# Kernel tuning notes

Measured on AMD Instinct MI355X. Metric: run time of the kernel, lower is better.

## Reference

```python
import jax, jax.numpy as jnp
import numpy as np

# pywt db2 analysis filters, reversed as in pytorch_wavelets.prep_filt_afb1d
# (torch conv1d is cross-correlation, so reversed filter == true convolution)
_H0 = np.array([0.48296291314469025, 0.8365163037378079,
                0.22414386804185735, -0.12940952255092145], dtype=np.float32)  # lowpass
_H1 = np.array([-0.12940952255092145, -0.22414386804185735,
                0.8365163037378079, -0.48296291314469025], dtype=np.float32)   # highpass


def setup_inputs() -> dict:
    key = jax.random.key(0)
    x = jax.random.normal(key, (16, 256, 128, 128), dtype=jnp.float32)
    return {"x": x}


def _dwt_channel(x):
    """1-level db2 DWT (mode='zero') along channel axis of x: (B, C, H, W).

    Equivalent to looping DWT1DForward over every (h, w) pixel, keeping the
    first C//2 low-pass coeffs in channels [:C//2] and the first C//2
    high-pass coeffs in channels [C//2:].
    """
    B, C, H, W = x.shape
    h0 = jnp.asarray(_H0, dtype=x.dtype)
    h1 = jnp.asarray(_H1, dtype=x.dtype)
    xt = jnp.moveaxis(x, 1, -1)                       # (B, H, W, C)
    # zero-mode padding: L=4, even C -> pad 2 each side (p = 4)
    xp = jnp.pad(xt, ((0, 0), (0, 0), (0, 0), (2, 2)))
    # output coeff k uses xp[..., 2k + t], t = 0..3; keep k = 0..C//2-1
    def filt(h):
        return sum(h[t] * jax.lax.slice_in_dim(xp, t, t + C - 1, stride=2, axis=3)
                   for t in range(4))                 # (B, H, W, C//2)
    lo = filt(h0)
    hi = filt(h1)
    out = jnp.concatenate([lo, hi], axis=-1)          # (B, H, W, C)
    return jnp.moveaxis(out, -1, 1)                   # (B, C, H, W)


def reference(x):
    return _dwt_channel(x)
```

## Files before the change

kernel.cpp:

```cpp
#include <hip/hip_runtime.h>

#define H00  0.48296291314469025f
#define H01  0.8365163037378079f
#define H02  0.22414386804185735f
#define H03 -0.12940952255092145f

#define H10 -0.12940952255092145f
#define H11 -0.22414386804185735f
#define H12  0.8365163037378079f
#define H13 -0.48296291314469025f

typedef float f4 __attribute__((ext_vector_type(4)));

namespace {
constexpr int Bn      = 16;
constexpr int Cn      = 256;
constexpr int HWv     = (128 * 128) / 4;
constexpr int KPAIRS  = Cn / 2;
constexpr int KPC     = 16;
constexpr int NCHUNK  = KPAIRS / KPC;
constexpr unsigned SPATIAL4 = (unsigned)Bn * HWv;
}

__global__ __launch_bounds__(256, 8) void dwt_db2_channel_kernel(
    const f4* __restrict__ x, f4* __restrict__ out)
{
    const unsigned tid   = blockIdx.x * 256u + threadIdx.x;
    const unsigned s4    = tid & (SPATIAL4 - 1);
    const unsigned chunk = tid >> 16;
    const unsigned b     = s4 / HWv;
    const unsigned hw    = s4 & (HWv - 1);
    const int      k0    = chunk * KPC;

    const f4* __restrict__ xp  = x   + (size_t)b * Cn * HWv + hw
                                     + (size_t)(2 * k0) * HWv;
    f4*       __restrict__ olo = out + (size_t)b * Cn * HWv + hw
                                     + (size_t)k0 * HWv;
    f4*       __restrict__ ohi = olo + (size_t)KPAIRS * HWv;

    f4 w0, w1;
    if (chunk == 0) {
        w0 = (f4){0.f, 0.f, 0.f, 0.f};
        w1 = w0;
    } else {
        w0 = __builtin_nontemporal_load(xp - 2 * HWv);
        w1 = __builtin_nontemporal_load(xp - 1 * HWv);
    }

#pragma unroll 2
    for (int kk = 0; kk < KPC; ++kk) {
        const f4 w2 = __builtin_nontemporal_load(xp);
        const f4 w3 = __builtin_nontemporal_load(xp + HWv);
        xp += 2 * HWv;

        f4 lo = H00 * w0 + H01 * w1 + H02 * w2 + H03 * w3;
        f4 hi = H10 * w0 + H11 * w1 + H12 * w2 + H13 * w3;

        __builtin_nontemporal_store(lo, olo);
        __builtin_nontemporal_store(hi, ohi);
        olo += HWv;
        ohi += HWv;

        w0 = w2;
        w1 = w3;
    }
}

extern "C" void kernel_launch(void* const* d_in, const int* in_sizes, int n_in,
                              void* d_out, int out_size, void* d_ws, size_t ws_size,
                              hipStream_t stream) {
    (void)in_sizes; (void)n_in; (void)d_ws; (void)ws_size; (void)out_size;
    const f4* x   = (const f4*)d_in[0];
    f4*       out = (f4*)d_out;

    const unsigned total_threads = SPATIAL4 * NCHUNK;
    const unsigned block = 256;
    const unsigned grid  = total_threads / block;

    dwt_db2_channel_kernel<<<grid, block, 0, stream>>>(x, out);
}
```

Before: 420.5 us.

## Assign each block a whole batch-channel-chunk plane with multiple vectors per thread

Work is redistributed so each 1024-thread block covers a full 128x128 plane for one batch and an 8-pair channel chunk, with each thread handling four float4 columns. The grid shrinks to 256 blocks and chunk size halves, giving more independent loads in flight per thread and contiguous plane-wide access per iteration. The trade-off is a grid of only 256 large blocks, which may underfill the GPU's compute units, plus extra halo reads because chunks are smaller.

```diff
diff --git a/kernel.cpp b/kernel.cpp
--- a/kernel.cpp
+++ b/kernel.cpp
@@ -15,54 +15,66 @@
 namespace {
 constexpr int Bn      = 16;
 constexpr int Cn      = 256;
-constexpr int HWv     = (128 * 128) / 4;
-constexpr int KPAIRS  = Cn / 2;
-constexpr int KPC     = 16;
-constexpr int NCHUNK  = KPAIRS / KPC;
-constexpr unsigned SPATIAL4 = (unsigned)Bn * HWv;
+constexpr int PLANE4  = (128 * 128) / 4;
+constexpr int KPC     = 8;
+constexpr int CHUNKS  = (Cn / 2) / KPC;
+constexpr int THREADS = 1024;
+constexpr int JPT     = PLANE4 / THREADS;
 }
 
-__global__ __launch_bounds__(256, 8) void dwt_db2_channel_kernel(
+__global__ __launch_bounds__(THREADS, 4) void dwt_db2_channel_kernel(
     const f4* __restrict__ x, f4* __restrict__ out)
 {
-    const unsigned tid   = blockIdx.x * 256u + threadIdx.x;
-    const unsigned s4    = tid & (SPATIAL4 - 1);
-    const unsigned chunk = tid >> 16;
-    const unsigned b     = s4 / HWv;
-    const unsigned hw    = s4 & (HWv - 1);
+    const unsigned blk   = blockIdx.x;
+    const unsigned b     = blk >> 4;
+    const unsigned chunk = blk & 15u;
     const int      k0    = chunk * KPC;
+    const unsigned t     = threadIdx.x;
 
-    const f4* __restrict__ xp  = x   + (size_t)b * Cn * HWv + hw
-                                     + (size_t)(2 * k0) * HWv;
-    f4*       __restrict__ olo = out + (size_t)b * Cn * HWv + hw
-                                     + (size_t)k0 * HWv;
-    f4*       __restrict__ ohi = olo + (size_t)KPAIRS * HWv;
+    const f4* __restrict__ xp  = x   + (size_t)b * Cn * PLANE4
+                                     + (size_t)(2 * k0) * PLANE4 + t;
+    f4*       __restrict__ plo = out + (size_t)b * Cn * PLANE4
+                                     + (size_t)k0 * PLANE4 + t;
+    f4*       __restrict__ phi = plo + (size_t)(Cn / 2) * PLANE4;
 
-    f4 w0, w1;
+    f4 w0[JPT], w1[JPT];
     if (chunk == 0) {
-        w0 = (f4){0.f, 0.f, 0.f, 0.f};
-        w1 = w0;
+#pragma unroll
+        for (int j = 0; j < JPT; ++j) {
+            w0[j] = (f4){0.f, 0.f, 0.f, 0.f};
+            w1[j] = (f4){0.f, 0.f, 0.f, 0.f};
+        }
     } else {
-        w0 = __builtin_nontemporal_load(xp - 2 * HWv);
-        w1 = __builtin_nontemporal_load(xp - 1 * HWv);
+#pragma unroll
+        for (int j = 0; j < JPT; ++j)
+            w0[j] = __builtin_nontemporal_load(xp - 2 * PLANE4 + j * THREADS);
+#pragma unroll
+        for (int j = 0; j < JPT; ++j)
+            w1[j] = __builtin_nontemporal_load(xp - 1 * PLANE4 + j * THREADS);
     }
 
-#pragma unroll 2
+#pragma unroll 1
     for (int kk = 0; kk < KPC; ++kk) {
-        const f4 w2 = __builtin_nontemporal_load(xp);
-        const f4 w3 = __builtin_nontemporal_load(xp + HWv);
-        xp += 2 * HWv;
+        f4 w2[JPT], w3[JPT];
+#pragma unroll
+        for (int j = 0; j < JPT; ++j)
+            w2[j] = __builtin_nontemporal_load(xp + j * THREADS);
+#pragma unroll
+        for (int j = 0; j < JPT; ++j)
+            w3[j] = __builtin_nontemporal_load(xp + PLANE4 + j * THREADS);
+        xp += 2 * PLANE4;
 
-        f4 lo = H00 * w0 + H01 * w1 + H02 * w2 + H03 * w3;
-        f4 hi = H10 * w0 + H11 * w1 + H12 * w2 + H13 * w3;
-
-        __builtin_nontemporal_store(lo, olo);
-        __builtin_nontemporal_store(hi, ohi);
-        olo += HWv;
-        ohi += HWv;
-
-        w0 = w2;
-        w1 = w3;
+#pragma unroll
+        for (int j = 0; j < JPT; ++j) {
+            const f4 lo = H00 * w0[j] + H01 * w1[j] + H02 * w2[j] + H03 * w3[j];
+            const f4 hi = H10 * w0[j] + H11 * w1[j] + H12 * w2[j] + H13 * w3[j];
+            __builtin_nontemporal_store(lo, plo + j * THREADS);
+            __builtin_nontemporal_store(hi, phi + j * THREADS);
+            w0[j] = w2[j];
+            w1[j] = w3[j];
+        }
+        plo += PLANE4;
+        phi += PLANE4;
     }
 }
 
@@ -73,9 +85,6 @@
     const f4* x   = (const f4*)d_in[0];
     f4*       out = (f4*)d_out;
 
-    const unsigned total_threads = SPATIAL4 * NCHUNK;
-    const unsigned block = 256;
-    const unsigned grid  = total_threads / block;
-
-    dwt_db2_channel_kernel<<<grid, block, 0, stream>>>(x, out);
+    const unsigned grid = Bn * CHUNKS;
+    dwt_db2_channel_kernel<<<grid, THREADS, 0, stream>>>(x, out);
 }
```

Result: no change. 428.1 us (+1.8%).
